# Performance work log

Measured on AMD Instinct MI355X. Metric: run time of the kernel, lower is better.

## Reference

```python
import jax, jax.numpy as jnp
import numpy as np

B, T, C, H, D = 4, 1024, 1024, 16, 64  # batch, seq, n_embd, heads, head_size


def setup_inputs() -> dict:
    key = jax.random.key(0)
    ks = jax.random.split(key, 6)
    x = jax.random.normal(ks[0], (B, T, C), dtype=jnp.float32)
    s = 0.02
    Wq = jax.random.normal(ks[1], (H, C, D), dtype=jnp.float32) * s
    Wk = jax.random.normal(ks[2], (H, C, D), dtype=jnp.float32) * s
    Wv = jax.random.normal(ks[3], (H, C, D), dtype=jnp.float32) * s
    Wo = jax.random.normal(ks[4], (H * D, C), dtype=jnp.float32) * s
    bo = jnp.zeros((C,), dtype=jnp.float32)
    return {"x": x, "Wq": Wq, "Wk": Wk, "Wv": Wv, "Wo": Wo, "bo": bo}


def reference(x, Wq, Wk, Wv, Wo, bo):
    # per-head projections (bias=False Linears), all heads batched via einsum
    q = jnp.einsum("btc,hcd->bhtd", x, Wq)
    k = jnp.einsum("btc,hcd->bhtd", x, Wk)
    v = jnp.einsum("btc,hcd->bhtd", x, Wv)
    # scaled dot-product scores: [B,H,T,T]
    scale = 1.0 / jnp.sqrt(jnp.asarray(D, dtype=q.dtype))
    scores = jnp.einsum("bhtd,bhsd->bhts", q, k) * scale
    # causal mask (tril), masked_fill with -inf equivalent
    causal = jnp.tril(jnp.ones((T, T), dtype=bool))
    neg = jnp.finfo(scores.dtype).min
    scores = jnp.where(causal[None, None], scores, neg)
    att = jax.nn.softmax(scores, axis=-1)
    # weighted aggregation of values, then concat heads
    out = jnp.einsum("bhts,bhsd->bhtd", att, v)
    out = out.transpose(0, 2, 1, 3).reshape(B, T, H * D)
    # output projection
    return out @ Wo + bo
```

## Files before the change

### kernel.cpp

```cpp
#include <hip/hip_runtime.h>
#include <hip/hip_bf16.h>
#include <stdint.h>


typedef float f32x4 __attribute__((ext_vector_type(4)));
typedef __bf16 bf16x8 __attribute__((ext_vector_type(8)));
typedef __bf16 bf16x4 __attribute__((ext_vector_type(4)));

#define GAS __attribute__((address_space(1)))
#define LAS __attribute__((address_space(3)))

__global__ __launch_bounds__(256) void prep_kernel(
    const float* __restrict__ x, const float* __restrict__ Wq,
    const float* __restrict__ Wk, const float* __restrict__ Wv,
    const float* __restrict__ Wo, __bf16* __restrict__ xb,
    __bf16* __restrict__ wqkvT, __bf16* __restrict__ woT) {
  __shared__ float tile[64][65];
  int bx = blockIdx.x;
  if (bx < 4096) {
    int i = bx * 256 + threadIdx.x;
    float4 f = ((const float4*)x)[i];
    bf16x4 o;
    o[0] = (__bf16)f.x; o[1] = (__bf16)f.y; o[2] = (__bf16)f.z; o[3] = (__bf16)f.w;
    ((bf16x4*)xb)[i] = o;
    return;
  }
  int tx = threadIdx.x & 63, ty = threadIdx.x >> 6;
  if (bx < 4864) {
    bx -= 4096;
    int z = bx >> 4;
    int r0 = (bx & 15) * 64;
    const float* s = (z < 16 ? Wq : (z < 32 ? Wk : Wv)) + (size_t)(z & 15) * 65536;
    __bf16* d = wqkvT + (size_t)z * 65536;
#pragma unroll
    for (int rr = ty; rr < 64; rr += 4)
      tile[rr][tx] = s[(size_t)(r0 + rr) * 64 + tx];
    __syncthreads();
#pragma unroll
    for (int rr = ty; rr < 64; rr += 4)
      d[(size_t)rr * 1024 + (r0 + tx)] = (__bf16)tile[tx][rr];
  } else {
    bx -= 4864;
    int r0 = (bx & 15) * 64, c0 = (bx >> 4) * 64;
#pragma unroll
    for (int rr = ty; rr < 64; rr += 4)
      tile[rr][tx] = Wo[(size_t)(r0 + rr) * 1024 + (c0 + tx)];
    __syncthreads();
#pragma unroll
    for (int rr = ty; rr < 64; rr += 4)
      woT[(size_t)(c0 + rr) * 1024 + (r0 + tx)] = (__bf16)tile[tx][rr];
  }
}

template <int MODE>
__global__ __launch_bounds__(256) void gemm_bt_kernel(
    const __bf16* __restrict__ A, const __bf16* __restrict__ BT, int N,
    __bf16* __restrict__ qo, __bf16* __restrict__ ko, __bf16* __restrict__ vo,
    float* __restrict__ Cout, const float* __restrict__ bias) {
  constexpr int K = 1024;
  extern __shared__ __align__(16) char smem_raw[];
  __bf16* Ash = (__bf16*)smem_raw;
  __bf16* Bsh = Ash + 2 * 128 * 64;
  const int tid = threadIdx.x;
  const int wid = tid >> 6, lane = tid & 63;
  const int fr = lane & 15, fq = lane >> 4;
  const int m0 = blockIdx.x * 128, n0 = blockIdx.y * 128;
  const int wr = wid >> 1, wc = wid & 1;
  const int lrow8 = lane >> 3;
  const int sc = ((lane & 7) ^ lrow8) * 8;

  f32x4 acc[4][4] = {};

  auto stage = [&](int k0, int buf) {
#pragma unroll
    for (int j = 0; j < 4; ++j) {
      int cc = j * 4 + wid;
      int row = cc * 8 + lrow8;
      const __bf16* gA = A + (size_t)(m0 + row) * K + k0 + sc;
      const __bf16* gB = BT + (size_t)(n0 + row) * K + k0 + sc;
      __builtin_amdgcn_global_load_lds((const GAS void*)gA, (LAS void*)&Ash[buf * 8192 + cc * 512], 16, 0, 0);
      __builtin_amdgcn_global_load_lds((const GAS void*)gB, (LAS void*)&Bsh[buf * 8192 + cc * 512], 16, 0, 0);
    }
  };

  stage(0, 0);
  __syncthreads();
  int buf = 0;
  for (int k0 = 0; k0 < K; k0 += 64) {
    if (k0 + 64 < K) stage(k0 + 64, buf ^ 1);
#pragma unroll
    for (int kk = 0; kk < 2; ++kk) {
      const int ch = ((((kk << 2) | fq)) ^ (fr & 7)) * 8;
      bf16x8 af[4], bfr[4];
#pragma unroll
      for (int mi = 0; mi < 4; ++mi) {
        int r = wr * 64 + mi * 16 + fr;
        af[mi] = *(const bf16x8*)&Ash[buf * 8192 + r * 64 + ch];
      }
#pragma unroll
      for (int ni = 0; ni < 4; ++ni) {
        int r = wc * 64 + ni * 16 + fr;
        bfr[ni] = *(const bf16x8*)&Bsh[buf * 8192 + r * 64 + ch];
      }
      __builtin_amdgcn_s_setprio(1);
#pragma unroll
      for (int mi = 0; mi < 4; ++mi)
#pragma unroll
        for (int ni = 0; ni < 4; ++ni)
          acc[mi][ni] = __builtin_amdgcn_mfma_f32_16x16x32_bf16(af[mi], bfr[ni], acc[mi][ni], 0, 0, 0);
      __builtin_amdgcn_s_setprio(0);
    }
    __syncthreads();
    buf ^= 1;
  }

  if (MODE == 0 && (n0 >> 10) == 2) {
    __bf16* spill = (__bf16*)smem_raw;
#pragma unroll
    for (int mi = 0; mi < 4; ++mi)
#pragma unroll
      for (int ni = 0; ni < 4; ++ni) {
        int nl = wc * 64 + ni * 16 + fr;
        int ml = wr * 64 + mi * 16 + fq * 4;
        bf16x4 pk;
#pragma unroll
        for (int r = 0; r < 4; ++r) pk[r] = (__bf16)acc[mi][ni][r];
        *(bf16x4*)&spill[nl * 136 + ml] = pk;
      }
    __syncthreads();
    const int b = m0 >> 10, t0 = m0 & 1023;
    const int lrow = lane >> 4, lch = lane & 15;
#pragma unroll
    for (int i = 0; i < 8; ++i) {
      int nl = wid * 32 + i * 4 + lrow;
      bf16x8 v = *(const bf16x8*)&spill[nl * 136 + lch * 8];
      int nn = (n0 & 1023) + nl;
      *(bf16x8*)&vo[(((size_t)b * 16 + (nn >> 6)) * 64 + (nn & 63)) * 1024 + t0 + lch * 8] = v;
    }
    return;
  }

#pragma unroll
  for (int mi = 0; mi < 4; ++mi) {
#pragma unroll
    for (int ni = 0; ni < 4; ++ni) {
      int n = n0 + wc * 64 + ni * 16 + fr;
      int mb = m0 + wr * 64 + mi * 16 + fq * 4;
#pragma unroll
      for (int r = 0; r < 4; ++r) {
        int m = mb + r;
        float val = acc[mi][ni][r];
        if (MODE == 0) {
          int nl = n & 1023;
          int h = nl >> 6, dd = nl & 63;
          int b = m >> 10, t = m & 1023;
          if ((n >> 10) == 0) {
            qo[(((size_t)b * 16 + h) * 1024 + t) * 64 + dd] = (__bf16)(val * 0.125f);
          } else {
            ko[(((size_t)b * 16 + h) * 1024 + t) * 64 + dd] = (__bf16)val;
          }
        } else {
          Cout[(size_t)m * N + n] = val + bias[n];
        }
      }
    }
  }
}

__global__ __launch_bounds__(256) void attn_fwd_kernel(
    const __bf16* __restrict__ Q, const __bf16* __restrict__ Kg,
    const __bf16* __restrict__ Vt, __bf16* __restrict__ O) {
  __shared__ __align__(16) __bf16 Ksh[2][64 * 64];
  __shared__ __align__(16) __bf16 VTs[2][64 * 64];
  __shared__ __align__(16) __bf16 Psh[4][16 * 64];

  const int bid = blockIdx.x;
  const int qt = 15 - (bid >> 6);
  const int bh = bid & 63;
  const int b = bh >> 4, h = bh & 15;
  const size_t base = (size_t)bh * 1024 * 64;
  const int tid = threadIdx.x, wid = tid >> 6, lane = tid & 63;
  const int fr = lane & 15, fq = lane >> 4;
  const int q0 = qt * 64;

  bf16x8 qf[2];
  {
    int qr = q0 + wid * 16 + fr;
    qf[0] = *(const bf16x8*)&Q[base + (size_t)qr * 64 + fq * 8];
    qf[1] = *(const bf16x8*)&Q[base + (size_t)qr * 64 + 32 + fq * 8];
  }
  f32x4 oacc[4] = {};
  float m = -1e30f, l = 0.f;

  const int lrow8 = lane >> 3;
  const int schunk = (lane & 7) ^ lrow8;

  auto stage = [&](int st, int buf) {
    const int s0 = st * 64;
#pragma unroll
    for (int i = 0; i < 2; ++i) {
      int rowbase = i * 32 + wid * 8;
      int row = rowbase + lrow8;
      const __bf16* gK = Kg + base + (size_t)(s0 + row) * 64 + schunk * 8;
      __builtin_amdgcn_global_load_lds((const GAS void*)gK,
          (LAS void*)&Ksh[buf][rowbase * 64], 16, 0, 0);
      const __bf16* gV = Vt + base + (size_t)row * 1024 + s0 + schunk * 8;
      __builtin_amdgcn_global_load_lds((const GAS void*)gV,
          (LAS void*)&VTs[buf][rowbase * 64], 16, 0, 0);
    }
  };

  auto compute = [&](int buf, int s0, bool maskT) {
    f32x4 s[4];
    __builtin_amdgcn_s_setprio(1);
#pragma unroll
    for (int sf = 0; sf < 4; ++sf) {
      int row = sf * 16 + fr, rx = fr & 7;
      bf16x8 kf0 = *(const bf16x8*)&Ksh[buf][row * 64 + ((fq ^ rx) << 3)];
      f32x4 z = {};
      s[sf] = __builtin_amdgcn_mfma_f32_16x16x32_bf16(kf0, qf[0], z, 0, 0, 0);
      bf16x8 kf1 = *(const bf16x8*)&Ksh[buf][row * 64 + (((4 + fq) ^ rx) << 3)];
      s[sf] = __builtin_amdgcn_mfma_f32_16x16x32_bf16(kf1, qf[1], s[sf], 0, 0, 0);
    }
    __builtin_amdgcn_s_setprio(0);

    const int qg = q0 + wid * 16 + fr;
    float sv[4][4];
    float mx = -1e30f;
#pragma unroll
    for (int sf = 0; sf < 4; ++sf)
#pragma unroll
      for (int r = 0; r < 4; ++r) {
        float x = s[sf][r];
        if (maskT) { int sg = s0 + sf * 16 + fq * 4 + r; if (sg > qg) x = -1e30f; }
        sv[sf][r] = x;
        mx = fmaxf(mx, x);
      }
    mx = fmaxf(mx, __shfl_xor(mx, 16));
    mx = fmaxf(mx, __shfl_xor(mx, 32));
    if (__any(mx - m > 8.0f)) {
      float mnew = fmaxf(m, mx);
      float alpha = __expf(m - mnew);
      m = mnew;
      l *= alpha;
      float ar[4];
#pragma unroll
      for (int r = 0; r < 4; ++r) ar[r] = __shfl(alpha, (lane & 48) | (fq * 4 + r));
#pragma unroll
      for (int df = 0; df < 4; ++df)
#pragma unroll
        for (int r = 0; r < 4; ++r) oacc[df][r] *= ar[r];
    }
    float rs = 0.f;
#pragma unroll
    for (int sf = 0; sf < 4; ++sf) {
      bf16x4 pk;
#pragma unroll
      for (int r = 0; r < 4; ++r) {
        float p = __expf(sv[sf][r] - m);
        rs += p;
        pk[r] = (__bf16)p;
      }
      *(bf16x4*)&Psh[wid][fr * 64 + ((((sf << 1) | (fq >> 1)) ^ (fr & 7)) << 3) + ((fq & 1) << 2)] = pk;
    }
    rs += __shfl_xor(rs, 16);
    rs += __shfl_xor(rs, 32);
    l += rs;

    __builtin_amdgcn_s_setprio(1);
#pragma unroll
    for (int kk = 0; kk < 2; ++kk) {
      bf16x8 pf = *(const bf16x8*)&Psh[wid][fr * 64 + ((((kk << 2) | fq) ^ (fr & 7)) << 3)];
#pragma unroll
      for (int df = 0; df < 4; ++df) {
        int row = df * 16 + fr;
        bf16x8 vf = *(const bf16x8*)&VTs[buf][row * 64 + ((((kk << 2) | fq) ^ (fr & 7)) << 3)];
        oacc[df] = __builtin_amdgcn_mfma_f32_16x16x32_bf16(pf, vf, oacc[df], 0, 0, 0);
      }
    }
    __builtin_amdgcn_s_setprio(0);
  };

  stage(0, 0);
  __syncthreads();
  int cur = 0;
  for (int st = 0; st <= qt; ++st) {
    if (st < qt) stage(st + 1, cur ^ 1);
    compute(cur, st * 64, st == qt);
    __syncthreads();
    cur ^= 1;
  }

  float lr[4];
#pragma unroll
  for (int r = 0; r < 4; ++r) lr[r] = __shfl(l, (lane & 48) | (fq * 4 + r));
#pragma unroll
  for (int r = 0; r < 4; ++r) {
    float inv = 1.0f / lr[r];
    int t = q0 + wid * 16 + fq * 4 + r;
    size_t orow = ((size_t)b * 1024 + t) * 1024 + h * 64;
#pragma unroll
    for (int df = 0; df < 4; ++df)
      O[orow + df * 16 + fr] = (__bf16)(oacc[df][r] * inv);
  }
}

extern "C" void kernel_launch(void* const* d_in, const int* in_sizes, int n_in,
                              void* d_out, int out_size, void* d_ws, size_t ws_size,
                              hipStream_t stream) {
  const float* x  = (const float*)d_in[0];
  const float* Wq = (const float*)d_in[1];
  const float* Wk = (const float*)d_in[2];
  const float* Wv = (const float*)d_in[3];
  const float* Wo = (const float*)d_in[4];
  const float* bo = (const float*)d_in[5];
  float* out = (float*)d_out;

  __bf16* xb    = (__bf16*)d_ws;
  __bf16* wqkvT = xb + (size_t)4096 * 1024;
  __bf16* woT   = wqkvT + (size_t)3072 * 1024;
  __bf16* qb    = woT + (size_t)1024 * 1024;
  __bf16* kb    = qb + (size_t)4 * 16 * 1024 * 64;
  __bf16* vtb   = kb + (size_t)4 * 16 * 1024 * 64;
  __bf16* Ob    = vtb + (size_t)4 * 16 * 1024 * 64;

  prep_kernel<<<5120, 256, 0, stream>>>(x, Wq, Wk, Wv, Wo, xb, wqkvT, woT);

  gemm_bt_kernel<0><<<dim3(32, 24), 256, 65536, stream>>>(xb, wqkvT, 3072, qb, kb, vtb, nullptr, nullptr);

  attn_fwd_kernel<<<1024, 256, 0, stream>>>(qb, kb, vtb, Ob);

  gemm_bt_kernel<1><<<dim3(32, 8), 256, 65536, stream>>>(Ob, woT, 1024,
      nullptr, nullptr, nullptr, out, bo);
}
```

Measured before the change: 82.21 us.

## Switch GEMM to triple-buffered K=32 stages with explicit waitcnt pipelining

Reworks the bf16 GEMM main loop from a double-buffered 64-wide K tile into a three-stage ring of 32-wide K tiles. Loads run two stages ahead, with explicit vmcnt/lgkmcnt waits and raw barriers in place of __syncthreads, plus a new LDS swizzle for the narrower tile. Shared memory per block drops from 64KB to 48KB, which may allow more blocks per CU. The cost is twice as many loop iterations and barriers, and correctness now depends on the hand-counted vmcnt values.

```diff
diff --git a/kernel.cpp b/kernel.cpp
--- a/kernel.cpp
+++ b/kernel.cpp
@@ -58,61 +58,76 @@
     __bf16* __restrict__ qo, __bf16* __restrict__ ko, __bf16* __restrict__ vo,
     float* __restrict__ Cout, const float* __restrict__ bias) {
   constexpr int K = 1024;
+  constexpr int NIT = K / 32;
   extern __shared__ __align__(16) char smem_raw[];
   __bf16* Ash = (__bf16*)smem_raw;
-  __bf16* Bsh = Ash + 2 * 128 * 64;
+  __bf16* Bsh = Ash + 3 * 4096;
   const int tid = threadIdx.x;
   const int wid = tid >> 6, lane = tid & 63;
   const int fr = lane & 15, fq = lane >> 4;
   const int m0 = blockIdx.x * 128, n0 = blockIdx.y * 128;
   const int wr = wid >> 1, wc = wid & 1;
-  const int lrow8 = lane >> 3;
-  const int sc = ((lane & 7) ^ lrow8) * 8;
+  const int srow = lane >> 2;
+  const int scol = (((lane & 3) ^ ((lane >> 3) & 3))) * 8;
+  const int swz = ((fq ^ ((fr >> 1) & 3))) << 3;
 
   f32x4 acc[4][4] = {};
 
-  auto stage = [&](int k0, int buf) {
-#pragma unroll
-    for (int j = 0; j < 4; ++j) {
-      int cc = j * 4 + wid;
-      int row = cc * 8 + lrow8;
-      const __bf16* gA = A + (size_t)(m0 + row) * K + k0 + sc;
-      const __bf16* gB = BT + (size_t)(n0 + row) * K + k0 + sc;
-      __builtin_amdgcn_global_load_lds((const GAS void*)gA, (LAS void*)&Ash[buf * 8192 + cc * 512], 16, 0, 0);
-      __builtin_amdgcn_global_load_lds((const GAS void*)gB, (LAS void*)&Bsh[buf * 8192 + cc * 512], 16, 0, 0);
+  auto stage = [&](int k0, int b) {
+#pragma unroll
+    for (int i = 0; i < 2; ++i) {
+      int chunk = wid * 2 + i;
+      int row = chunk * 16 + srow;
+      const __bf16* gA = A + (size_t)(m0 + row) * K + k0 + scol;
+      const __bf16* gB = BT + (size_t)(n0 + row) * K + k0 + scol;
+      __builtin_amdgcn_global_load_lds((const GAS void*)gA, (LAS void*)&Ash[b * 4096 + chunk * 512], 16, 0, 0);
+      __builtin_amdgcn_global_load_lds((const GAS void*)gB, (LAS void*)&Bsh[b * 4096 + chunk * 512], 16, 0, 0);
     }
   };
 
   stage(0, 0);
+  stage(32, 1);
+  asm volatile("s_waitcnt vmcnt(4)" ::: "memory");
+  __builtin_amdgcn_s_barrier();
+  __builtin_amdgcn_sched_barrier(0);
+
+  int b = 0, bs = 2;
+  for (int it = 0; it < NIT; ++it) {
+    if (it + 2 < NIT) stage((it + 2) * 32, bs);
+    bf16x8 af[4], bfr[4];
+#pragma unroll
+    for (int mi = 0; mi < 4; ++mi) {
+      int r = wr * 64 + mi * 16 + fr;
+      af[mi] = *(const bf16x8*)&Ash[b * 4096 + r * 32 + swz];
+    }
+#pragma unroll
+    for (int ni = 0; ni < 4; ++ni) {
+      int r = wc * 64 + ni * 16 + fr;
+      bfr[ni] = *(const bf16x8*)&Bsh[b * 4096 + r * 32 + swz];
+    }
+    asm volatile("s_waitcnt lgkmcnt(0)" ::: "memory");
+    __builtin_amdgcn_sched_barrier(0);
+    __builtin_amdgcn_s_setprio(1);
+#pragma unroll
+    for (int mi = 0; mi < 4; ++mi)
+#pragma unroll
+      for (int ni = 0; ni < 4; ++ni)
+        acc[mi][ni] = __builtin_amdgcn_mfma_f32_16x16x32_bf16(af[mi], bfr[ni], acc[mi][ni], 0, 0, 0);
+    __builtin_amdgcn_s_setprio(0);
+    __builtin_amdgcn_sched_barrier(0);
+    if (it + 1 < NIT) {
+      if (it + 2 < NIT) {
+        asm volatile("s_waitcnt vmcnt(4)" ::: "memory");
+      } else {
+        asm volatile("s_waitcnt vmcnt(0)" ::: "memory");
+      }
+      __builtin_amdgcn_s_barrier();
+      __builtin_amdgcn_sched_barrier(0);
+    }
+    b = (b == 2) ? 0 : b + 1;
+    bs = (bs == 2) ? 0 : bs + 1;
+  }
   __syncthreads();
-  int buf = 0;
-  for (int k0 = 0; k0 < K; k0 += 64) {
-    if (k0 + 64 < K) stage(k0 + 64, buf ^ 1);
-#pragma unroll
-    for (int kk = 0; kk < 2; ++kk) {
-      const int ch = ((((kk << 2) | fq)) ^ (fr & 7)) * 8;
-      bf16x8 af[4], bfr[4];
-#pragma unroll
-      for (int mi = 0; mi < 4; ++mi) {
-        int r = wr * 64 + mi * 16 + fr;
-        af[mi] = *(const bf16x8*)&Ash[buf * 8192 + r * 64 + ch];
-      }
-#pragma unroll
-      for (int ni = 0; ni < 4; ++ni) {
-        int r = wc * 64 + ni * 16 + fr;
-        bfr[ni] = *(const bf16x8*)&Bsh[buf * 8192 + r * 64 + ch];
-      }
-      __builtin_amdgcn_s_setprio(1);
-#pragma unroll
-      for (int mi = 0; mi < 4; ++mi)
-#pragma unroll
-        for (int ni = 0; ni < 4; ++ni)
-          acc[mi][ni] = __builtin_amdgcn_mfma_f32_16x16x32_bf16(af[mi], bfr[ni], acc[mi][ni], 0, 0, 0);
-      __builtin_amdgcn_s_setprio(0);
-    }
-    __syncthreads();
-    buf ^= 1;
-  }
 
   if (MODE == 0 && (n0 >> 10) == 2) {
     __bf16* spill = (__bf16*)smem_raw;
@@ -128,14 +143,14 @@
         *(bf16x4*)&spill[nl * 136 + ml] = pk;
       }
     __syncthreads();
-    const int b = m0 >> 10, t0 = m0 & 1023;
+    const int bb = m0 >> 10, t0 = m0 & 1023;
     const int lrow = lane >> 4, lch = lane & 15;
 #pragma unroll
     for (int i = 0; i < 8; ++i) {
       int nl = wid * 32 + i * 4 + lrow;
       bf16x8 v = *(const bf16x8*)&spill[nl * 136 + lch * 8];
       int nn = (n0 & 1023) + nl;
-      *(bf16x8*)&vo[(((size_t)b * 16 + (nn >> 6)) * 64 + (nn & 63)) * 1024 + t0 + lch * 8] = v;
+      *(bf16x8*)&vo[(((size_t)bb * 16 + (nn >> 6)) * 64 + (nn & 63)) * 1024 + t0 + lch * 8] = v;
     }
     return;
   }
@@ -153,11 +168,11 @@
         if (MODE == 0) {
           int nl = n & 1023;
           int h = nl >> 6, dd = nl & 63;
-          int b = m >> 10, t = m & 1023;
+          int bb = m >> 10, t = m & 1023;
           if ((n >> 10) == 0) {
-            qo[(((size_t)b * 16 + h) * 1024 + t) * 64 + dd] = (__bf16)(val * 0.125f);
+            qo[(((size_t)bb * 16 + h) * 1024 + t) * 64 + dd] = (__bf16)(val * 0.125f);
           } else {
-            ko[(((size_t)b * 16 + h) * 1024 + t) * 64 + dd] = (__bf16)val;
+            ko[(((size_t)bb * 16 + h) * 1024 + t) * 64 + dd] = (__bf16)val;
           }
         } else {
           Cout[(size_t)m * N + n] = val + bias[n];
@@ -326,10 +341,10 @@
 
   prep_kernel<<<5120, 256, 0, stream>>>(x, Wq, Wk, Wv, Wo, xb, wqkvT, woT);
 
-  gemm_bt_kernel<0><<<dim3(32, 24), 256, 65536, stream>>>(xb, wqkvT, 3072, qb, kb, vtb, nullptr, nullptr);
+  gemm_bt_kernel<0><<<dim3(32, 24), 256, 49152, stream>>>(xb, wqkvT, 3072, qb, kb, vtb, nullptr, nullptr);
 
   attn_fwd_kernel<<<1024, 256, 0, stream>>>(qb, kb, vtb, Ob);
 
-  gemm_bt_kernel<1><<<dim3(32, 8), 256, 65536, stream>>>(Ob, woT, 1024,
+  gemm_bt_kernel<1><<<dim3(32, 8), 256, 49152, stream>>>(Ob, woT, 1024,
       nullptr, nullptr, nullptr, out, bo);
 }
```

After: 86.06 us. +4.7%, slower.
